# Optimization experiments

Measured on AMD Instinct MI355X. Metric: run time of the kernel, lower is better.

## Reference

```python
import jax, jax.numpy as jnp
import numpy as np

DIM = 1024
H = 16
HD = DIM // H  # 64
SCALE = HD ** -0.5
EPS = 1e-5


def setup_inputs() -> dict:
    key = jax.random.key(0)
    ks = jax.random.split(key, 8)
    B, N = 2, 2048
    x = jax.random.normal(ks[0], (B, N, DIM), dtype=jnp.float32)
    qkv_w = jax.random.normal(ks[1], (5 * DIM, DIM), dtype=jnp.float32) * (DIM ** -0.5)
    proj_w = jax.random.normal(ks[2], (DIM, DIM), dtype=jnp.float32) * (DIM ** -0.5)
    proj_b = jnp.zeros((DIM,), dtype=jnp.float32)
    lambda_q1 = jax.random.normal(ks[3], (HD,), dtype=jnp.float32) * 0.1
    lambda_k1 = jax.random.normal(ks[4], (HD,), dtype=jnp.float32) * 0.1
    lambda_q2 = jax.random.normal(ks[5], (HD,), dtype=jnp.float32) * 0.1
    lambda_k2 = jax.random.normal(ks[6], (HD,), dtype=jnp.float32) * 0.1
    return {"x": x, "qkv_w": qkv_w, "proj_w": proj_w, "proj_b": proj_b,
            "lambda_q1": lambda_q1, "lambda_k1": lambda_k1,
            "lambda_q2": lambda_q2, "lambda_k2": lambda_k2}


def reference(x, qkv_w, proj_w, proj_b, lambda_q1, lambda_k1, lambda_q2, lambda_k2):
    B, N, C = x.shape
    # qkv projection -> (5, B, H, N, hd)
    qkv = jnp.einsum('bnc,fc->bnf', x, qkv_w).reshape(B, N, 5, H, HD)
    qkv = jnp.transpose(qkv, (2, 0, 3, 1, 4))
    q1, q2, k1, k2, v = qkv[0], qkv[1], qkv[2], qkv[3], qkv[4]
    # dual attention score matrices (B, H, N, N)
    attn1 = jax.nn.softmax(jnp.einsum('bhqd,bhkd->bhqk', q1, k1) * SCALE, axis=-1)
    attn2 = jax.nn.softmax(jnp.einsum('bhqd,bhkd->bhqk', q2, k2) * SCALE, axis=-1)
    lambda_full = (jnp.exp(jnp.sum(lambda_q1 * lambda_k1))
                   - jnp.exp(jnp.sum(lambda_q2 * lambda_k2)) + 0.8)
    attn = attn1 - lambda_full * attn2
    out = jnp.einsum('bhqk,bhkd->bhqd', attn, v)  # (B,H,N,hd)
    out = jnp.transpose(out, (0, 2, 1, 3)).reshape(B, N, C)
    # RMSNorm (no affine) over last dim, then fixed scale (1 - 0.8)
    out = out * jax.lax.rsqrt(jnp.mean(out * out, axis=-1, keepdims=True) + EPS)
    out = out * (1.0 - 0.8)
    return jnp.einsum('bnc,oc->bno', out, proj_w) + proj_b
```

## Files before the change

### kernel.cpp

```cpp
#include <hip/hip_runtime.h>
#include <hip/hip_bf16.h>

#define SEQ   2048
#define BATCH 2
#define NHEAD 16
#define HDIM  64
#define CDIM  1024
#define QKV_F 5120
#define SCALE 0.125f
#define LOG2E 1.44269504f
#define EPSV  1e-5f

typedef __bf16 bf16;
typedef __bf16 bf16x4 __attribute__((ext_vector_type(4)));
typedef __bf16 bf16x8 __attribute__((ext_vector_type(8)));
typedef float  f32x4  __attribute__((ext_vector_type(4)));
typedef float  f32x16 __attribute__((ext_vector_type(16)));

#define MFMA16(a, b, c) __builtin_amdgcn_mfma_f32_16x16x32_bf16(a, b, c, 0, 0, 0)
#define MFMA32(a, b, c) __builtin_amdgcn_mfma_f32_32x32x16_bf16(a, b, c, 0, 0, 0)

__device__ __forceinline__ unsigned pkbf(float a, float b) {
    union { bf16 h[2]; unsigned u; } t;
    t.h[0] = (bf16)a; t.h[1] = (bf16)b;
    return t.u;
}
__device__ __forceinline__ unsigned short bfbits(float a) {
    union { bf16 h; unsigned short u; } t;
    t.h = (bf16)a;
    return t.u;
}
__device__ __forceinline__ void gload16(const void* g, void* l) {
    __builtin_amdgcn_global_load_lds(
        (const __attribute__((address_space(1))) unsigned int*)g,
        (__attribute__((address_space(3))) unsigned int*)l, 16, 0, 0);
}

__global__ __launch_bounds__(256) void cvt_bf16(
    const float* __restrict__ s, bf16* __restrict__ d)
{
    const int i = (blockIdx.x * 256 + threadIdx.x) * 8;
    float4 a = *(const float4*)(s + i);
    float4 b = *(const float4*)(s + i + 4);
    bf16x8 t;
    t[0] = (bf16)a.x; t[1] = (bf16)a.y; t[2] = (bf16)a.z; t[3] = (bf16)a.w;
    t[4] = (bf16)b.x; t[5] = (bf16)b.y; t[6] = (bf16)b.z; t[7] = (bf16)b.w;
    *(bf16x8*)(d + i) = t;
}

template <int EPI>
__global__ __launch_bounds__(256) void gemm_lds(
    const bf16* __restrict__ A, const bf16* __restrict__ Bw,
    const float* __restrict__ bias,
    bf16* __restrict__ outq, float* __restrict__ outp,
    int M, int Nn, int K)
{
    __shared__ __align__(16) bf16 As[128 * 64];
    __shared__ __align__(16) bf16 Bs[128 * 64];

    const int tid  = threadIdx.x;
    const int lane = tid & 63;
    const int wave = tid >> 6;
    const int wr = wave >> 1, wc = wave & 1;
    const int g = lane >> 4, fr = lane & 15;
    const int m0 = blockIdx.y * 128;
    const int n0 = blockIdx.x * 128;

    const int lrow = lane >> 3;
    const int lcol = (lane & 7) << 3;

    f32x4 acc[4][4];
#pragma unroll
    for (int m = 0; m < 4; ++m)
#pragma unroll
        for (int n = 0; n < 4; ++n) acc[m][n] = f32x4{0.f, 0.f, 0.f, 0.f};

    const int nkt = K >> 6;
    for (int kt = 0; kt < nkt; ++kt) {
        const int k0 = kt << 6;
        __syncthreads();
#pragma unroll
        for (int i = 0; i < 4; ++i) {
            const int chunk = wave * 4 + i;
            const int row = chunk * 8 + lrow;
            gload16(A + (size_t)(m0 + row) * K + k0 + lcol, As + chunk * 512);
            gload16(Bw + (size_t)(n0 + row) * K + k0 + lcol, Bs + chunk * 512);
        }
        __syncthreads();
#pragma unroll
        for (int ks = 0; ks < 2; ++ks) {
            bf16x8 af[4], bfr[4];
#pragma unroll
            for (int m = 0; m < 4; ++m)
                af[m] = *(const bf16x8*)(As + (wr * 64 + m * 16 + fr) * 64 + ks * 32 + g * 8);
#pragma unroll
            for (int n = 0; n < 4; ++n)
                bfr[n] = *(const bf16x8*)(Bs + (wc * 64 + n * 16 + fr) * 64 + ks * 32 + g * 8);
#pragma unroll
            for (int m = 0; m < 4; ++m)
#pragma unroll
                for (int n = 0; n < 4; ++n)
                    acc[m][n] = MFMA16(af[m], bfr[n], acc[m][n]);
        }
    }

#pragma unroll
    for (int m = 0; m < 4; ++m) {
#pragma unroll
        for (int n = 0; n < 4; ++n) {
            const int row0 = m0 + wr * 64 + m * 16 + g * 4;
            const int col  = n0 + wc * 64 + n * 16 + fr;
            if (EPI == 0) {
                const int bb = row0 >> 11, nn = row0 & (SEQ - 1);
                const int sI = col >> 10, rem = col & (CDIM - 1);
                const int hh = rem >> 6, dd = rem & 63;
                const size_t base = ((size_t)((sI * BATCH + bb) * NHEAD + hh)) << 17;
                if (sI == 4) {
                    ushort4 u;
                    u.x = bfbits(acc[m][n][0]);
                    u.y = bfbits(acc[m][n][1]);
                    u.z = bfbits(acc[m][n][2]);
                    u.w = bfbits(acc[m][n][3]);
                    *(ushort4*)(outq + base + ((size_t)dd << 11) + nn) = u;
                } else {
                    const float sc = (sI < 2) ? SCALE * LOG2E : 1.f;
#pragma unroll
                    for (int r = 0; r < 4; ++r)
                        outq[base + ((size_t)(nn + r) << 6) + dd] = (bf16)(acc[m][n][r] * sc);
                }
            } else {
#pragma unroll
                for (int r = 0; r < 4; ++r)
                    outp[(size_t)(row0 + r) * Nn + col] = acc[m][n][r] + bias[col];
            }
        }
    }
}

__device__ __forceinline__ void attn_state(
    const char* __restrict__ Ks, const bf16x8* qf, const bf16x8 (*vf)[2],
    int lq, int hi, int s32,
    f32x16& oa, f32x16& ob, float& mS, float& lS)
{
    f32x16 s;
#pragma unroll
    for (int r = 0; r < 16; ++r) s[r] = 0.f;
    const int krow = s32 * 32 + lq;
    const int ksw  = (krow & 7) << 4;
#pragma unroll
    for (int ks = 0; ks < 4; ++ks) {
        bf16x8 kf = *(const bf16x8*)(Ks + krow * 128 + ((ks * 32 + hi * 16) ^ ksw));
        s = MFMA32(kf, qf[ks], s);
    }
    float pm = s[0];
#pragma unroll
    for (int r = 1; r < 16; ++r) pm = fmaxf(pm, s[r]);
    pm = fmaxf(pm, __shfl_xor(pm, 32));
    if (!__all(pm <= mS + 8.f * LOG2E)) {
        float mn = fmaxf(mS, pm);
        float alpha = __builtin_amdgcn_exp2f(mS - mn);
        lS *= alpha;
        oa *= alpha;
        ob *= alpha;
        mS = mn;
    }
    float p[16];
    float rs = 0.f;
#pragma unroll
    for (int r = 0; r < 16; ++r) { p[r] = __builtin_amdgcn_exp2f(s[r] - mS); rs += p[r]; }
    rs += __shfl_xor(rs, 32);
    lS += rs;
#pragma unroll
    for (int s16 = 0; s16 < 2; ++s16) {
        unsigned X = pkbf(p[s16 * 8 + 0], p[s16 * 8 + 1]);
        unsigned Z = pkbf(p[s16 * 8 + 2], p[s16 * 8 + 3]);
        unsigned Y = pkbf(p[s16 * 8 + 4], p[s16 * 8 + 5]);
        unsigned W = pkbf(p[s16 * 8 + 6], p[s16 * 8 + 7]);
        auto xy = __builtin_amdgcn_permlane32_swap(X, Y, false, false);
        auto zw = __builtin_amdgcn_permlane32_swap(Z, W, false, false);
        union { unsigned u[4]; bf16x8 v; } pf;
        pf.u[0] = xy[0]; pf.u[1] = zw[0]; pf.u[2] = xy[1]; pf.u[3] = zw[1];
        oa = MFMA32(vf[0][s16], pf.v, oa);
        ob = MFMA32(vf[1][s16], pf.v, ob);
    }
}

__global__ __launch_bounds__(512, 2) void diff_attn(
    const bf16* __restrict__ qkv,
    const float* __restrict__ lq1, const float* __restrict__ lk1,
    const float* __restrict__ lq2, const float* __restrict__ lk2,
    float* __restrict__ attn_out)
{
    __shared__ __align__(16) char K1s[64 * 128];
    __shared__ __align__(16) char K2s[64 * 128];
    __shared__ __align__(16) char Vts[64 * 128];

    const int tid = threadIdx.x;
    const int lane = tid & 63, wave = tid >> 6;
    const int lq = lane & 31, hi = lane >> 5;
    const int bh = blockIdx.y, b = bh >> 4, h = bh & 15;
    const int q0w = blockIdx.x * 256 + wave * 32;

    float ls1 = 0.f, ls2 = 0.f;
    for (int i = 0; i < HDIM; ++i) { ls1 += lq1[i] * lk1[i]; ls2 += lq2[i] * lk2[i]; }
    const float lam = __expf(ls1) - __expf(ls2) + 0.8f;

    const size_t HS = (size_t)SEQ * HDIM;
    const char* q1p = (const char*)(qkv + ((size_t)((0 * BATCH + b) * NHEAD + h)) * HS);
    const char* q2p = (const char*)(qkv + ((size_t)((1 * BATCH + b) * NHEAD + h)) * HS);
    const char* k1p = (const char*)(qkv + ((size_t)((2 * BATCH + b) * NHEAD + h)) * HS);
    const char* k2p = (const char*)(qkv + ((size_t)((3 * BATCH + b) * NHEAD + h)) * HS);
    const char* vtp = (const char*)(qkv + ((size_t)((4 * BATCH + b) * NHEAD + h)) * HS);

    bf16x8 qf1[4], qf2[4];
#pragma unroll
    for (int ks = 0; ks < 4; ++ks) {
        qf1[ks] = *(const bf16x8*)(q1p + (size_t)(q0w + lq) * 128 + ks * 32 + hi * 16);
        qf2[ks] = *(const bf16x8*)(q2p + (size_t)(q0w + lq) * 128 + ks * 32 + hi * 16);
    }

    f32x16 o1a, o1b, o2a, o2b;
#pragma unroll
    for (int r = 0; r < 16; ++r) { o1a[r] = 0.f; o1b[r] = 0.f; o2a[r] = 0.f; o2b[r] = 0.f; }
    float m1 = -1e30f, l1 = 0.f, m2 = -1e30f, l2 = 0.f;

    const int srow = tid >> 3;
    const int sc   = (tid & 7) << 4;
    const int swc  = sc ^ ((srow & 7) << 4);

    for (int kt = 0; kt < SEQ / 64; ++kt) {
        __syncthreads();
        uint4 ka = *(const uint4*)(k1p + (size_t)(kt * 64 + srow) * 128 + sc);
        uint4 kb = *(const uint4*)(k2p + (size_t)(kt * 64 + srow) * 128 + sc);
        uint4 vv = *(const uint4*)(vtp + (size_t)srow * (SEQ * 2) + kt * 128 + sc);
        *(uint4*)(K1s + srow * 128 + swc) = ka;
        *(uint4*)(K2s + srow * 128 + swc) = kb;
        *(uint4*)(Vts + srow * 128 + swc) = vv;
        __syncthreads();

#pragma unroll
        for (int s32 = 0; s32 < 2; ++s32) {
            bf16x8 vf[2][2];
#pragma unroll
            for (int dt = 0; dt < 2; ++dt) {
                const int vrow = dt * 32 + lq;
                const int vsw  = (vrow & 7) << 4;
#pragma unroll
                for (int s16 = 0; s16 < 2; ++s16)
                    vf[dt][s16] = *(const bf16x8*)(Vts + vrow * 128 +
                                   ((s32 * 64 + s16 * 32 + hi * 16) ^ vsw));
            }
            attn_state(K1s, qf1, vf, lq, hi, s32, o1a, o1b, m1, l1);
            attn_state(K2s, qf2, vf, lq, hi, s32, o2a, o2b, m2, l2);
        }
    }

    const float i1 = 1.f / l1;
    const float i2 = lam / l2;
    const int nq = q0w + lq;
    float* op = attn_out + ((size_t)(b * SEQ + nq)) * CDIM + h * HDIM;
#pragma unroll
    for (int dt = 0; dt < 2; ++dt) {
        const f32x16& a1 = dt ? o1b : o1a;
        const f32x16& a2 = dt ? o2b : o2a;
#pragma unroll
        for (int rq = 0; rq < 4; ++rq) {
            const int d0 = dt * 32 + rq * 8 + hi * 4;
            float4 o;
            o.x = a1[rq * 4 + 0] * i1 - i2 * a2[rq * 4 + 0];
            o.y = a1[rq * 4 + 1] * i1 - i2 * a2[rq * 4 + 1];
            o.z = a1[rq * 4 + 2] * i1 - i2 * a2[rq * 4 + 2];
            o.w = a1[rq * 4 + 3] * i1 - i2 * a2[rq * 4 + 3];
            *(float4*)(op + d0) = o;
        }
    }
}

__global__ __launch_bounds__(256) void rmsnorm_bf16(
    const float* __restrict__ in, bf16* __restrict__ out)
{
    __shared__ float red[4];
    const int row = blockIdx.x, tid = threadIdx.x;
    const float4 v = ((const float4*)(in + (size_t)row * CDIM))[tid];
    float ss = v.x * v.x + v.y * v.y + v.z * v.z + v.w * v.w;
#pragma unroll
    for (int m = 1; m < 64; m <<= 1) ss += __shfl_xor(ss, m);
    if ((tid & 63) == 0) red[tid >> 6] = ss;
    __syncthreads();
    float tot = red[0] + red[1] + red[2] + red[3];
    float sc = rsqrtf(tot * (1.f / CDIM) + EPSV) * 0.2f;
    bf16x4 o;
    o[0] = (bf16)(v.x * sc); o[1] = (bf16)(v.y * sc);
    o[2] = (bf16)(v.z * sc); o[3] = (bf16)(v.w * sc);
    ((bf16x4*)(out + (size_t)row * CDIM))[tid] = o;
}

extern "C" void kernel_launch(void* const* d_in, const int* in_sizes, int n_in,
                              void* d_out, int out_size, void* d_ws, size_t ws_size,
                              hipStream_t stream)
{
    (void)in_sizes; (void)n_in; (void)out_size; (void)ws_size;
    const float* x      = (const float*)d_in[0];
    const float* qkv_w  = (const float*)d_in[1];
    const float* proj_w = (const float*)d_in[2];
    const float* proj_b = (const float*)d_in[3];
    const float* lq1    = (const float*)d_in[4];
    const float* lk1    = (const float*)d_in[5];
    const float* lq2    = (const float*)d_in[6];
    const float* lk2    = (const float*)d_in[7];
    float* out = (float*)d_out;

    char* ws = (char*)d_ws;
    bf16*  qkv_t    = (bf16*)ws;
    bf16*  attn_b   = (bf16*)ws;
    float* attn_out = (float*)(ws + (size_t)40 * 1024 * 1024);
    bf16*  x_b      = (bf16*)(ws + (size_t)40 * 1024 * 1024);
    bf16*  qkvw_b   = (bf16*)(ws + (size_t)56 * 1024 * 1024);
    bf16*  projw_b  = (bf16*)(ws + (size_t)66 * 1024 * 1024);

    dim3 blk(256);
    cvt_bf16<<<dim3((BATCH * SEQ * CDIM) / 2048), blk, 0, stream>>>(x, x_b);
    cvt_bf16<<<dim3((QKV_F * CDIM) / 2048), blk, 0, stream>>>(qkv_w, qkvw_b);
    cvt_bf16<<<dim3((CDIM * CDIM) / 2048), blk, 0, stream>>>(proj_w, projw_b);
    gemm_lds<0><<<dim3(QKV_F / 128, (BATCH * SEQ) / 128), blk, 0, stream>>>(
        x_b, qkvw_b, nullptr, qkv_t, nullptr, BATCH * SEQ, QKV_F, CDIM);
    diff_attn<<<dim3(SEQ / 256, BATCH * NHEAD), dim3(512), 0, stream>>>(
        qkv_t, lq1, lk1, lq2, lk2, attn_out);
    rmsnorm_bf16<<<dim3(BATCH * SEQ), blk, 0, stream>>>(attn_out, attn_b);
    gemm_lds<1><<<dim3(CDIM / 128, (BATCH * SEQ) / 128), blk, 0, stream>>>(
        attn_b, projw_b, proj_b, nullptr, out, BATCH * SEQ, CDIM, CDIM);
}
```

Measured before the change: 226.4 us.

## Split KV range across two wave groups in diff attention and merge via LDS

The attention block now covers 128 queries, and its two 4-wave groups each process half of the key/value sequence. The partial softmax states are then merged through shared memory, which doubles the grid size to raise occupancy and parallelism. K/V tiles are loaded with a gload16 helper (likely a direct global-to-LDS load). The change also adds s_setprio around the MFMAs, tree reductions for max and sum, and raises the launch-bounds occupancy target to 4. The risks are extra merge synchronisation, more LDS per block, and register pressure under the tighter launch bound.

Measured after the change: 395.9 us. 1.75x slower.

```diff
diff --git a/kernel.cpp b/kernel.cpp
--- a/kernel.cpp
+++ b/kernel.cpp
@@ -147,14 +147,19 @@
     for (int r = 0; r < 16; ++r) s[r] = 0.f;
     const int krow = s32 * 32 + lq;
     const int ksw  = (krow & 7) << 4;
+    __builtin_amdgcn_s_setprio(1);
 #pragma unroll
     for (int ks = 0; ks < 4; ++ks) {
         bf16x8 kf = *(const bf16x8*)(Ks + krow * 128 + ((ks * 32 + hi * 16) ^ ksw));
         s = MFMA32(kf, qf[ks], s);
     }
-    float pm = s[0];
-#pragma unroll
-    for (int r = 1; r < 16; ++r) pm = fmaxf(pm, s[r]);
+    __builtin_amdgcn_s_setprio(0);
+    float t0 = fmaxf(s[0], s[1]),  t1 = fmaxf(s[2], s[3]);
+    float t2 = fmaxf(s[4], s[5]),  t3 = fmaxf(s[6], s[7]);
+    float t4 = fmaxf(s[8], s[9]),  t5 = fmaxf(s[10], s[11]);
+    float t6 = fmaxf(s[12], s[13]), t7 = fmaxf(s[14], s[15]);
+    t0 = fmaxf(t0, t4); t1 = fmaxf(t1, t5); t2 = fmaxf(t2, t6); t3 = fmaxf(t3, t7);
+    float pm = fmaxf(fmaxf(t0, t2), fmaxf(t1, t3));
     pm = fmaxf(pm, __shfl_xor(pm, 32));
     if (!__all(pm <= mS + 8.f * LOG2E)) {
         float mn = fmaxf(mS, pm);
@@ -164,42 +169,52 @@
         ob *= alpha;
         mS = mn;
     }
-    float p[16];
-    float rs = 0.f;
-#pragma unroll
-    for (int r = 0; r < 16; ++r) { p[r] = __builtin_amdgcn_exp2f(s[r] - mS); rs += p[r]; }
+#pragma unroll
+    for (int r = 0; r < 16; ++r) s[r] = __builtin_amdgcn_exp2f(s[r] - mS);
+    float u0 = s[0] + s[1],  u1 = s[2] + s[3];
+    float u2 = s[4] + s[5],  u3 = s[6] + s[7];
+    float u4 = s[8] + s[9],  u5 = s[10] + s[11];
+    float u6 = s[12] + s[13], u7 = s[14] + s[15];
+    u0 += u4; u1 += u5; u2 += u6; u3 += u7;
+    float rs = (u0 + u2) + (u1 + u3);
     rs += __shfl_xor(rs, 32);
     lS += rs;
 #pragma unroll
     for (int s16 = 0; s16 < 2; ++s16) {
-        unsigned X = pkbf(p[s16 * 8 + 0], p[s16 * 8 + 1]);
-        unsigned Z = pkbf(p[s16 * 8 + 2], p[s16 * 8 + 3]);
-        unsigned Y = pkbf(p[s16 * 8 + 4], p[s16 * 8 + 5]);
-        unsigned W = pkbf(p[s16 * 8 + 6], p[s16 * 8 + 7]);
+        unsigned X = pkbf(s[s16 * 8 + 0], s[s16 * 8 + 1]);
+        unsigned Z = pkbf(s[s16 * 8 + 2], s[s16 * 8 + 3]);
+        unsigned Y = pkbf(s[s16 * 8 + 4], s[s16 * 8 + 5]);
+        unsigned W = pkbf(s[s16 * 8 + 6], s[s16 * 8 + 7]);
         auto xy = __builtin_amdgcn_permlane32_swap(X, Y, false, false);
         auto zw = __builtin_amdgcn_permlane32_swap(Z, W, false, false);
         union { unsigned u[4]; bf16x8 v; } pf;
         pf.u[0] = xy[0]; pf.u[1] = zw[0]; pf.u[2] = xy[1]; pf.u[3] = zw[1];
+        __builtin_amdgcn_s_setprio(1);
         oa = MFMA32(vf[0][s16], pf.v, oa);
         ob = MFMA32(vf[1][s16], pf.v, ob);
-    }
-}
-
-__global__ __launch_bounds__(512, 2) void diff_attn(
+        __builtin_amdgcn_s_setprio(0);
+    }
+}
+
+__global__ __launch_bounds__(512, 4) void diff_attn(
     const bf16* __restrict__ qkv,
     const float* __restrict__ lq1, const float* __restrict__ lk1,
     const float* __restrict__ lq2, const float* __restrict__ lk2,
     float* __restrict__ attn_out)
 {
-    __shared__ __align__(16) char K1s[64 * 128];
-    __shared__ __align__(16) char K2s[64 * 128];
-    __shared__ __align__(16) char Vts[64 * 128];
+    __shared__ __align__(16) char SMEM[49152];
 
     const int tid = threadIdx.x;
     const int lane = tid & 63, wave = tid >> 6;
+    const int wg = wave & 3, grp = wave >> 2;
     const int lq = lane & 31, hi = lane >> 5;
     const int bh = blockIdx.y, b = bh >> 4, h = bh & 15;
-    const int q0w = blockIdx.x * 256 + wave * 32;
+    const int q0w = blockIdx.x * 128 + wg * 32;
+    const int kv0 = grp * (SEQ / 2);
+
+    char* Ks1 = SMEM + grp * 24576;
+    char* Ks2 = Ks1 + 8192;
+    char* Vts = Ks1 + 16384;
 
     float ls1 = 0.f, ls2 = 0.f;
     for (int i = 0; i < HDIM; ++i) { ls1 += lq1[i] * lk1[i]; ls2 += lq2[i] * lk2[i]; }
@@ -224,18 +239,26 @@
     for (int r = 0; r < 16; ++r) { o1a[r] = 0.f; o1b[r] = 0.f; o2a[r] = 0.f; o2b[r] = 0.f; }
     float m1 = -1e30f, l1 = 0.f, m2 = -1e30f, l2 = 0.f;
 
-    const int srow = tid >> 3;
-    const int sc   = (tid & 7) << 4;
-    const int swc  = sc ^ ((srow & 7) << 4);
-
-    for (int kt = 0; kt < SEQ / 64; ++kt) {
+    const int lrow8 = lane >> 3;
+    const int scol  = ((lane & 7) ^ lrow8) << 4;
+
+    for (int kt = 0; kt < SEQ / 2 / 64; ++kt) {
         __syncthreads();
-        uint4 ka = *(const uint4*)(k1p + (size_t)(kt * 64 + srow) * 128 + sc);
-        uint4 kb = *(const uint4*)(k2p + (size_t)(kt * 64 + srow) * 128 + sc);
-        uint4 vv = *(const uint4*)(vtp + (size_t)srow * (SEQ * 2) + kt * 128 + sc);
-        *(uint4*)(K1s + srow * 128 + swc) = ka;
-        *(uint4*)(K2s + srow * 128 + swc) = kb;
-        *(uint4*)(Vts + srow * 128 + swc) = vv;
+#pragma unroll
+        for (int i = 0; i < 6; ++i) {
+            const int c = wg * 6 + i;
+            const int tile = c >> 3, ch = c & 7;
+            const int row = ch * 8 + lrow8;
+            char* ldst = Ks1 + tile * 8192 + ch * 1024;
+            const char* src;
+            if (tile < 2) {
+                const char* kb = tile ? k2p : k1p;
+                src = kb + (size_t)(kv0 + kt * 64 + row) * 128 + scol;
+            } else {
+                src = vtp + (size_t)row * (SEQ * 2) + (size_t)(kv0 + kt * 64) * 2 + scol;
+            }
+            gload16(src, ldst);
+        }
         __syncthreads();
 
 #pragma unroll
@@ -250,28 +273,78 @@
                     vf[dt][s16] = *(const bf16x8*)(Vts + vrow * 128 +
                                    ((s32 * 64 + s16 * 32 + hi * 16) ^ vsw));
             }
-            attn_state(K1s, qf1, vf, lq, hi, s32, o1a, o1b, m1, l1);
-            attn_state(K2s, qf2, vf, lq, hi, s32, o2a, o2b, m2, l2);
-        }
-    }
-
-    const float i1 = 1.f / l1;
-    const float i2 = lam / l2;
-    const int nq = q0w + lq;
-    float* op = attn_out + ((size_t)(b * SEQ + nq)) * CDIM + h * HDIM;
-#pragma unroll
-    for (int dt = 0; dt < 2; ++dt) {
-        const f32x16& a1 = dt ? o1b : o1a;
-        const f32x16& a2 = dt ? o2b : o2a;
-#pragma unroll
-        for (int rq = 0; rq < 4; ++rq) {
-            const int d0 = dt * 32 + rq * 8 + hi * 4;
-            float4 o;
-            o.x = a1[rq * 4 + 0] * i1 - i2 * a2[rq * 4 + 0];
-            o.y = a1[rq * 4 + 1] * i1 - i2 * a2[rq * 4 + 1];
-            o.z = a1[rq * 4 + 2] * i1 - i2 * a2[rq * 4 + 2];
-            o.w = a1[rq * 4 + 3] * i1 - i2 * a2[rq * 4 + 3];
-            *(float4*)(op + d0) = o;
+            attn_state(Ks1, qf1, vf, lq, hi, s32, o1a, o1b, m1, l1);
+            attn_state(Ks2, qf2, vf, lq, hi, s32, o2a, o2b, m2, l2);
+        }
+    }
+
+    float* MF = (float*)SMEM;
+    float* OF = (float*)(SMEM + 4096);
+    const int mbase = wg * 64 + lane;
+
+    __syncthreads();
+    if (grp == 1) {
+        MF[0 * 256 + mbase] = m1;
+        MF[1 * 256 + mbase] = l1;
+        MF[2 * 256 + mbase] = m2;
+        MF[3 * 256 + mbase] = l2;
+#pragma unroll
+        for (int r = 0; r < 16; ++r) {
+            OF[r * 256 + mbase]        = o1a[r];
+            OF[(16 + r) * 256 + mbase] = o1b[r];
+        }
+    }
+    __syncthreads();
+    float aA1, aB1, aA2, aB2;
+    if (grp == 0) {
+        const float mB1 = MF[0 * 256 + mbase], lB1 = MF[1 * 256 + mbase];
+        const float mB2 = MF[2 * 256 + mbase], lB2 = MF[3 * 256 + mbase];
+        const float mn1 = fmaxf(m1, mB1), mn2 = fmaxf(m2, mB2);
+        aA1 = __builtin_amdgcn_exp2f(m1 - mn1);
+        aB1 = __builtin_amdgcn_exp2f(mB1 - mn1);
+        aA2 = __builtin_amdgcn_exp2f(m2 - mn2);
+        aB2 = __builtin_amdgcn_exp2f(mB2 - mn2);
+        l1 = l1 * aA1 + lB1 * aB1;
+        l2 = l2 * aA2 + lB2 * aB2;
+#pragma unroll
+        for (int r = 0; r < 16; ++r) {
+            o1a[r] = o1a[r] * aA1 + OF[r * 256 + mbase] * aB1;
+            o1b[r] = o1b[r] * aA1 + OF[(16 + r) * 256 + mbase] * aB1;
+        }
+    }
+    __syncthreads();
+    if (grp == 1) {
+#pragma unroll
+        for (int r = 0; r < 16; ++r) {
+            OF[r * 256 + mbase]        = o2a[r];
+            OF[(16 + r) * 256 + mbase] = o2b[r];
+        }
+    }
+    __syncthreads();
+    if (grp == 0) {
+#pragma unroll
+        for (int r = 0; r < 16; ++r) {
+            o2a[r] = o2a[r] * aA2 + OF[r * 256 + mbase] * aB2;
+            o2b[r] = o2b[r] * aA2 + OF[(16 + r) * 256 + mbase] * aB2;
+        }
+        const float i1 = 1.f / l1;
+        const float i2 = lam / l2;
+        const int nq = q0w + lq;
+        float* op = attn_out + ((size_t)(b * SEQ + nq)) * CDIM + h * HDIM;
+#pragma unroll
+        for (int dt = 0; dt < 2; ++dt) {
+            const f32x16& a1 = dt ? o1b : o1a;
+            const f32x16& a2 = dt ? o2b : o2a;
+#pragma unroll
+            for (int rq = 0; rq < 4; ++rq) {
+                const int d0 = dt * 32 + rq * 8 + hi * 4;
+                float4 o;
+                o.x = a1[rq * 4 + 0] * i1 - i2 * a2[rq * 4 + 0];
+                o.y = a1[rq * 4 + 1] * i1 - i2 * a2[rq * 4 + 1];
+                o.z = a1[rq * 4 + 2] * i1 - i2 * a2[rq * 4 + 2];
+                o.w = a1[rq * 4 + 3] * i1 - i2 * a2[rq * 4 + 3];
+                *(float4*)(op + d0) = o;
+            }
         }
     }
 }
@@ -324,7 +397,7 @@
     cvt_bf16<<<dim3((CDIM * CDIM) / 2048), blk, 0, stream>>>(proj_w, projw_b);
     gemm_lds<0><<<dim3(QKV_F / 128, (BATCH * SEQ) / 128), blk, 0, stream>>>(
         x_b, qkvw_b, nullptr, qkv_t, nullptr, BATCH * SEQ, QKV_F, CDIM);
-    diff_attn<<<dim3(SEQ / 256, BATCH * NHEAD), dim3(512), 0, stream>>>(
+    diff_attn<<<dim3(SEQ / 128, BATCH * NHEAD), dim3(512), 0, stream>>>(
         qkv_t, lq1, lk1, lq2, lk2, attn_out);
     rmsnorm_bf16<<<dim3(BATCH * SEQ), blk, 0, stream>>>(attn_out, attn_b);
     gemm_lds<1><<<dim3(CDIM / 128, (BATCH * SEQ) / 128), blk, 0, stream>>>(
```

## Restructure diff attention to 16x16 MFMA tiles with smaller blocks and async K loads

Applied to the files above, without the earlier changes.

Rewrites the differential attention kernel to use 16x16x32 MFMAs with 16 query rows per wave and 64 queries per 256-thread block, replacing the 32x32 tile scheme with 32 rows per wave and 512 threads. K tiles are now loaded directly into LDS with global_load_lds, and V is gathered in a permuted order so the softmax probabilities feed the PV MFMA without permlane swaps. The grid is reordered so heads vary fastest, and s_setprio hints are placed around the MFMA sections. The smaller per-block query tile means K/V tiles are reloaded by four times as many blocks, trading more L2 traffic for higher occupancy and parallelism.

New measurement: 229.7 us. Within noise of the previous version (+1.4%).

```diff
diff --git a/kernel.cpp b/kernel.cpp
--- a/kernel.cpp
+++ b/kernel.cpp
@@ -15,10 +15,8 @@
 typedef __bf16 bf16x4 __attribute__((ext_vector_type(4)));
 typedef __bf16 bf16x8 __attribute__((ext_vector_type(8)));
 typedef float  f32x4  __attribute__((ext_vector_type(4)));
-typedef float  f32x16 __attribute__((ext_vector_type(16)));
 
 #define MFMA16(a, b, c) __builtin_amdgcn_mfma_f32_16x16x32_bf16(a, b, c, 0, 0, 0)
-#define MFMA32(a, b, c) __builtin_amdgcn_mfma_f32_32x32x16_bf16(a, b, c, 0, 0, 0)
 
 __device__ __forceinline__ unsigned pkbf(float a, float b) {
     union { bf16 h[2]; unsigned u; } t;
@@ -137,69 +135,21 @@
     }
 }
 
-__device__ __forceinline__ void attn_state(
-    const char* __restrict__ Ks, const bf16x8* qf, const bf16x8 (*vf)[2],
-    int lq, int hi, int s32,
-    f32x16& oa, f32x16& ob, float& mS, float& lS)
-{
-    f32x16 s;
-#pragma unroll
-    for (int r = 0; r < 16; ++r) s[r] = 0.f;
-    const int krow = s32 * 32 + lq;
-    const int ksw  = (krow & 7) << 4;
-#pragma unroll
-    for (int ks = 0; ks < 4; ++ks) {
-        bf16x8 kf = *(const bf16x8*)(Ks + krow * 128 + ((ks * 32 + hi * 16) ^ ksw));
-        s = MFMA32(kf, qf[ks], s);
-    }
-    float pm = s[0];
-#pragma unroll
-    for (int r = 1; r < 16; ++r) pm = fmaxf(pm, s[r]);
-    pm = fmaxf(pm, __shfl_xor(pm, 32));
-    if (!__all(pm <= mS + 8.f * LOG2E)) {
-        float mn = fmaxf(mS, pm);
-        float alpha = __builtin_amdgcn_exp2f(mS - mn);
-        lS *= alpha;
-        oa *= alpha;
-        ob *= alpha;
-        mS = mn;
-    }
-    float p[16];
-    float rs = 0.f;
-#pragma unroll
-    for (int r = 0; r < 16; ++r) { p[r] = __builtin_amdgcn_exp2f(s[r] - mS); rs += p[r]; }
-    rs += __shfl_xor(rs, 32);
-    lS += rs;
-#pragma unroll
-    for (int s16 = 0; s16 < 2; ++s16) {
-        unsigned X = pkbf(p[s16 * 8 + 0], p[s16 * 8 + 1]);
-        unsigned Z = pkbf(p[s16 * 8 + 2], p[s16 * 8 + 3]);
-        unsigned Y = pkbf(p[s16 * 8 + 4], p[s16 * 8 + 5]);
-        unsigned W = pkbf(p[s16 * 8 + 6], p[s16 * 8 + 7]);
-        auto xy = __builtin_amdgcn_permlane32_swap(X, Y, false, false);
-        auto zw = __builtin_amdgcn_permlane32_swap(Z, W, false, false);
-        union { unsigned u[4]; bf16x8 v; } pf;
-        pf.u[0] = xy[0]; pf.u[1] = zw[0]; pf.u[2] = xy[1]; pf.u[3] = zw[1];
-        oa = MFMA32(vf[0][s16], pf.v, oa);
-        ob = MFMA32(vf[1][s16], pf.v, ob);
-    }
-}
-
-__global__ __launch_bounds__(512, 2) void diff_attn(
+__global__ __launch_bounds__(256, 4) void diff_attn(
     const bf16* __restrict__ qkv,
     const float* __restrict__ lq1, const float* __restrict__ lk1,
     const float* __restrict__ lq2, const float* __restrict__ lk2,
     float* __restrict__ attn_out)
 {
-    __shared__ __align__(16) char K1s[64 * 128];
-    __shared__ __align__(16) char K2s[64 * 128];
-    __shared__ __align__(16) char Vts[64 * 128];
+    __shared__ __align__(16) char K1s[8192];
+    __shared__ __align__(16) char K2s[8192];
+    __shared__ __align__(16) char Vts[8192];
 
     const int tid = threadIdx.x;
     const int lane = tid & 63, wave = tid >> 6;
-    const int lq = lane & 31, hi = lane >> 5;
-    const int bh = blockIdx.y, b = bh >> 4, h = bh & 15;
-    const int q0w = blockIdx.x * 256 + wave * 32;
+    const int g = lane >> 4, fr = lane & 15;
+    const int bh = blockIdx.x, b = bh >> 4, h = bh & 15;
+    const int q0 = blockIdx.y * 64 + wave * 16;
 
     float ls1 = 0.f, ls2 = 0.f;
     for (int i = 0; i < HDIM; ++i) { ls1 += lq1[i] * lk1[i]; ls2 += lq2[i] * lk2[i]; }
@@ -212,67 +162,135 @@
     const char* k2p = (const char*)(qkv + ((size_t)((3 * BATCH + b) * NHEAD + h)) * HS);
     const char* vtp = (const char*)(qkv + ((size_t)((4 * BATCH + b) * NHEAD + h)) * HS);
 
-    bf16x8 qf1[4], qf2[4];
-#pragma unroll
-    for (int ks = 0; ks < 4; ++ks) {
-        qf1[ks] = *(const bf16x8*)(q1p + (size_t)(q0w + lq) * 128 + ks * 32 + hi * 16);
-        qf2[ks] = *(const bf16x8*)(q2p + (size_t)(q0w + lq) * 128 + ks * 32 + hi * 16);
-    }
-
-    f32x16 o1a, o1b, o2a, o2b;
-#pragma unroll
-    for (int r = 0; r < 16; ++r) { o1a[r] = 0.f; o1b[r] = 0.f; o2a[r] = 0.f; o2b[r] = 0.f; }
+    bf16x8 qf1[2], qf2[2];
+#pragma unroll
+    for (int ks = 0; ks < 2; ++ks) {
+        qf1[ks] = *(const bf16x8*)(q1p + (size_t)(q0 + fr) * 128 + ks * 64 + g * 16);
+        qf2[ks] = *(const bf16x8*)(q2p + (size_t)(q0 + fr) * 128 + ks * 64 + g * 16);
+    }
+
+    f32x4 o1[4], o2[4];
+#pragma unroll
+    for (int d = 0; d < 4; ++d) { o1[d] = f32x4{0, 0, 0, 0}; o2[d] = f32x4{0, 0, 0, 0}; }
     float m1 = -1e30f, l1 = 0.f, m2 = -1e30f, l2 = 0.f;
 
-    const int srow = tid >> 3;
-    const int sc   = (tid & 7) << 4;
-    const int swc  = sc ^ ((srow & 7) << 4);
+    const int lrow8 = lane >> 3;
+    const int scol  = ((lane & 7) ^ lrow8) << 4;
+    const int vd = tid >> 2;
+    const char* vsrc = vtp + (size_t)vd * (SEQ * 2);
+    char* vdst = Vts + vd * 128;
+    const int vswz = (vd & 7) << 4;
+
+    auto qk_sm = [&](const char* Ks, const bf16x8* qf, f32x4* o,
+                     float& mS, float& lS, unsigned* pw) {
+        f32x4 s0{0, 0, 0, 0}, s1{0, 0, 0, 0}, s2{0, 0, 0, 0}, s3{0, 0, 0, 0};
+        __builtin_amdgcn_s_setprio(1);
+#pragma unroll
+        for (int ks = 0; ks < 2; ++ks) {
+            const int c = (ks * 64 + g * 16);
+            bf16x8 k0 = *(const bf16x8*)(Ks + (0 * 16 + fr) * 128 + (c ^ ((fr & 7) << 4)));
+            bf16x8 k1 = *(const bf16x8*)(Ks + (1 * 16 + fr) * 128 + (c ^ ((fr & 7) << 4)));
+            bf16x8 k2 = *(const bf16x8*)(Ks + (2 * 16 + fr) * 128 + (c ^ ((fr & 7) << 4)));
+            bf16x8 k3 = *(const bf16x8*)(Ks + (3 * 16 + fr) * 128 + (c ^ ((fr & 7) << 4)));
+            s0 = MFMA16(k0, qf[ks], s0);
+            s1 = MFMA16(k1, qf[ks], s1);
+            s2 = MFMA16(k2, qf[ks], s2);
+            s3 = MFMA16(k3, qf[ks], s3);
+        }
+        __builtin_amdgcn_s_setprio(0);
+        f32x4 t01 = __builtin_elementwise_max(s0, s1);
+        f32x4 t23 = __builtin_elementwise_max(s2, s3);
+        f32x4 t = __builtin_elementwise_max(t01, t23);
+        float pm = fmaxf(fmaxf(t[0], t[1]), fmaxf(t[2], t[3]));
+        pm = fmaxf(pm, __shfl_xor(pm, 16));
+        pm = fmaxf(pm, __shfl_xor(pm, 32));
+        if (!__all(pm <= mS + 8.f * LOG2E)) {
+            float mn = fmaxf(mS, pm);
+            float alpha = __builtin_amdgcn_exp2f(mS - mn);
+            lS *= alpha;
+#pragma unroll
+            for (int d = 0; d < 4; ++d) o[d] *= alpha;
+            mS = mn;
+        }
+#pragma unroll
+        for (int r = 0; r < 4; ++r) {
+            s0[r] = __builtin_amdgcn_exp2f(s0[r] - mS);
+            s1[r] = __builtin_amdgcn_exp2f(s1[r] - mS);
+            s2[r] = __builtin_amdgcn_exp2f(s2[r] - mS);
+            s3[r] = __builtin_amdgcn_exp2f(s3[r] - mS);
+        }
+        f32x4 u01 = (s0 + s1) + (s2 + s3);
+        float rs = (u01[0] + u01[1]) + (u01[2] + u01[3]);
+        rs += __shfl_xor(rs, 16);
+        rs += __shfl_xor(rs, 32);
+        lS += rs;
+        pw[0] = pkbf(s0[0], s0[1]); pw[1] = pkbf(s0[2], s0[3]);
+        pw[2] = pkbf(s1[0], s1[1]); pw[3] = pkbf(s1[2], s1[3]);
+        pw[4] = pkbf(s2[0], s2[1]); pw[5] = pkbf(s2[2], s2[3]);
+        pw[6] = pkbf(s3[0], s3[1]); pw[7] = pkbf(s3[2], s3[3]);
+    };
 
     for (int kt = 0; kt < SEQ / 64; ++kt) {
+        const int kvb = kt * 64;
         __syncthreads();
-        uint4 ka = *(const uint4*)(k1p + (size_t)(kt * 64 + srow) * 128 + sc);
-        uint4 kb = *(const uint4*)(k2p + (size_t)(kt * 64 + srow) * 128 + sc);
-        uint4 vv = *(const uint4*)(vtp + (size_t)srow * (SEQ * 2) + kt * 128 + sc);
-        *(uint4*)(K1s + srow * 128 + swc) = ka;
-        *(uint4*)(K2s + srow * 128 + swc) = kb;
-        *(uint4*)(Vts + srow * 128 + swc) = vv;
+#pragma unroll
+        for (int i = 0; i < 4; ++i) {
+            const int c = wave * 4 + i;
+            const int t = c >> 3, ch = c & 7;
+            const char* kb = t ? k2p : k1p;
+            gload16(kb + (size_t)(kvb + ch * 8 + lrow8) * 128 + scol,
+                    (t ? K2s : K1s) + ch * 1024);
+        }
+        uint2 vv[4];
+#pragma unroll
+        for (int i = 0; i < 4; ++i) {
+            const int u = (tid & 3) * 4 + i;
+            const int G = u >> 3, gg = (u >> 1) & 3, jh = u & 1;
+            const int kvrun = 8 * G + 4 * jh + gg;
+            vv[i] = *(const uint2*)(vsrc + (size_t)(kvb + kvrun * 4) * 2);
+        }
+#pragma unroll
+        for (int i = 0; i < 4; ++i) {
+            const int u = (tid & 3) * 4 + i;
+            *(uint2*)(vdst + ((u * 8) ^ vswz)) = vv[i];
+        }
         __syncthreads();
 
-#pragma unroll
-        for (int s32 = 0; s32 < 2; ++s32) {
-            bf16x8 vf[2][2];
-#pragma unroll
-            for (int dt = 0; dt < 2; ++dt) {
-                const int vrow = dt * 32 + lq;
-                const int vsw  = (vrow & 7) << 4;
-#pragma unroll
-                for (int s16 = 0; s16 < 2; ++s16)
-                    vf[dt][s16] = *(const bf16x8*)(Vts + vrow * 128 +
-                                   ((s32 * 64 + s16 * 32 + hi * 16) ^ vsw));
+        unsigned p1w[8], p2w[8];
+        qk_sm(K1s, qf1, o1, m1, l1, p1w);
+        qk_sm(K2s, qf2, o2, m2, l2, p2w);
+
+        __builtin_amdgcn_s_setprio(1);
+#pragma unroll
+        for (int G = 0; G < 2; ++G) {
+            union { unsigned u[4]; bf16x8 v; } pf1, pf2;
+            pf1.u[0] = p1w[G * 4 + 0]; pf1.u[1] = p1w[G * 4 + 1];
+            pf1.u[2] = p1w[G * 4 + 2]; pf1.u[3] = p1w[G * 4 + 3];
+            pf2.u[0] = p2w[G * 4 + 0]; pf2.u[1] = p2w[G * 4 + 1];
+            pf2.u[2] = p2w[G * 4 + 2]; pf2.u[3] = p2w[G * 4 + 3];
+#pragma unroll
+            for (int ds = 0; ds < 4; ++ds) {
+                const int vrow = ds * 16 + fr;
+                bf16x8 vf = *(const bf16x8*)(Vts + vrow * 128 +
+                              ((G * 64 + g * 16) ^ ((vrow & 7) << 4)));
+                o1[ds] = MFMA16(vf, pf1.v, o1[ds]);
+                o2[ds] = MFMA16(vf, pf2.v, o2[ds]);
             }
-            attn_state(K1s, qf1, vf, lq, hi, s32, o1a, o1b, m1, l1);
-            attn_state(K2s, qf2, vf, lq, hi, s32, o2a, o2b, m2, l2);
-        }
+        }
+        __builtin_amdgcn_s_setprio(0);
     }
 
     const float i1 = 1.f / l1;
     const float i2 = lam / l2;
-    const int nq = q0w + lq;
-    float* op = attn_out + ((size_t)(b * SEQ + nq)) * CDIM + h * HDIM;
-#pragma unroll
-    for (int dt = 0; dt < 2; ++dt) {
-        const f32x16& a1 = dt ? o1b : o1a;
-        const f32x16& a2 = dt ? o2b : o2a;
-#pragma unroll
-        for (int rq = 0; rq < 4; ++rq) {
-            const int d0 = dt * 32 + rq * 8 + hi * 4;
-            float4 o;
-            o.x = a1[rq * 4 + 0] * i1 - i2 * a2[rq * 4 + 0];
-            o.y = a1[rq * 4 + 1] * i1 - i2 * a2[rq * 4 + 1];
-            o.z = a1[rq * 4 + 2] * i1 - i2 * a2[rq * 4 + 2];
-            o.w = a1[rq * 4 + 3] * i1 - i2 * a2[rq * 4 + 3];
-            *(float4*)(op + d0) = o;
-        }
+    float* op = attn_out + ((size_t)(b * SEQ + q0 + fr)) * CDIM + h * HDIM;
+#pragma unroll
+    for (int ds = 0; ds < 4; ++ds) {
+        float4 o;
+        o.x = o1[ds][0] * i1 - i2 * o2[ds][0];
+        o.y = o1[ds][1] * i1 - i2 * o2[ds][1];
+        o.z = o1[ds][2] * i1 - i2 * o2[ds][2];
+        o.w = o1[ds][3] * i1 - i2 * o2[ds][3];
+        *(float4*)(op + ds * 16 + g * 4) = o;
     }
 }
 
@@ -324,7 +342,7 @@
     cvt_bf16<<<dim3((CDIM * CDIM) / 2048), blk, 0, stream>>>(proj_w, projw_b);
     gemm_lds<0><<<dim3(QKV_F / 128, (BATCH * SEQ) / 128), blk, 0, stream>>>(
         x_b, qkvw_b, nullptr, qkv_t, nullptr, BATCH * SEQ, QKV_F, CDIM);
-    diff_attn<<<dim3(SEQ / 256, BATCH * NHEAD), dim3(512), 0, stream>>>(
+    diff_attn<<<dim3(BATCH * NHEAD, SEQ / 64), blk, 0, stream>>>(
         qkv_t, lq1, lk1, lq2, lk2, attn_out);
     rmsnorm_bf16<<<dim3(BATCH * SEQ), blk, 0, stream>>>(attn_out, attn_b);
     gemm_lds<1><<<dim3(CDIM / 128, (BATCH * SEQ) / 128), blk, 0, stream>>>(
```
